# Kernel tuning notes

Hardware: AMD Instinct MI355X
Metric: run time of the kernel (lower is better)

The kernel has to match this reference:

```python
import jax, jax.numpy as jnp
import numpy as np

B, N, D = 8, 1024, 768
H, Z = 12, 64          # num_heads, head_dim (D = H*Z)
HID = 3072             # int(D * mlp_ratio)


def setup_inputs() -> dict:
    key = jax.random.key(0)
    k1, k2, k3, k4 = jax.random.split(key, 4)
    s = 0.02
    x = jax.random.normal(k1, (B, N, D), dtype=jnp.float32)
    Wq = jax.random.normal(k2, (D, D), dtype=jnp.float32) * s
    Wk = jax.random.normal(k3, (D, D), dtype=jnp.float32) * s
    betas = jnp.full((H,), Z ** -0.5, dtype=jnp.float32)
    W_mlp = jax.random.normal(k4, (HID, D), dtype=jnp.float32) * s
    return {"x": x, "Wq": Wq, "Wk": Wk, "betas": betas, "W_mlp": W_mlp}


def reference(x, Wq, Wk, betas, W_mlp):
    # --- KQ-aligned attention ---
    # torch Linear: y = x @ W.T ; weight shape [out=D, in=D]
    Q = jnp.einsum('bnd,ed->bne', x, Wq).reshape(B, N, H, Z).transpose(0, 2, 1, 3)  # bhqz
    K = jnp.einsum('bnd,ed->bne', x, Wk).reshape(B, N, H, Z).transpose(0, 2, 1, 3)  # bhkz
    Wq_r = Wq.reshape(H, Z, D)
    Wk_r = Wk.reshape(H, Z, D)
    F1 = jnp.einsum('hzd,bhkz->bkhd', Wq_r, K)
    F2 = jnp.einsum('hzd,bhqz->bqhd', Wk_r, Q)
    scores = jnp.einsum('bhqz,bhkz,h->bhqk', Q, K, betas)
    attn = jax.nn.softmax(scores, axis=-1)
    T1 = jnp.einsum('bkhd,bhqk->bqd', F1, attn)
    T2 = jnp.einsum('bqhd,bhqk->bkd', F2, attn)
    # --- symmetric-weight Hopfield MLP (bias=False) ---
    hid = jax.nn.relu(jnp.einsum('bnd,hd->bnh', x, W_mlp))
    mlp = jnp.einsum('bnh,hd->bnd', hid, W_mlp)
    return T1 + T2 + mlp
```

## Files before the change

### kernel.cpp

```cpp
#include <hip/hip_runtime.h>
#include <hip/hip_bf16.h>

#define Bq 8
#define Nq 1024
#define Dq 768
#define Hq 12
#define Zq 64
#define HIDq 3072
#define BN (Bq*Nq)
#define QKP 1536

typedef unsigned short u16;
typedef short s16x8 __attribute__((ext_vector_type(8)));
typedef float f32x4 __attribute__((ext_vector_type(4)));
typedef unsigned short u16x4 __attribute__((ext_vector_type(4)));

#define MFMA16 __builtin_amdgcn_mfma_f32_16x16x32_bf16
#define GLOAD16(g, l) __builtin_amdgcn_global_load_lds( \
    (const __attribute__((address_space(1))) void*)(const void*)(g), \
    (__attribute__((address_space(3))) void*)(l), 16, 0, 0)

__device__ __forceinline__ u16 f2bf(float f) {
  unsigned u = __float_as_uint(f);
  return (u16)((u + 0x7FFFu + ((u >> 16) & 1u)) >> 16);
}

__device__ __forceinline__ unsigned pk2bf(float a, float b) {
  union { __hip_bfloat162 h; unsigned u; } cv;
  cv.h.x = __float2bfloat16(a);
  cv.h.y = __float2bfloat16(b);
  return cv.u;
}

__device__ __forceinline__ void xcd_swizzle(int gx, int gy, int& bx, int& by) {
  int l = blockIdx.y * gx + blockIdx.x;
  int c = l & 7, j = l >> 3;
  by = c * (gy >> 3) + j / gx;
  bx = j % gx;
}

__global__ __launch_bounds__(256) void cvt2(const float* __restrict__ x, u16* __restrict__ xb,
                                            const float* __restrict__ Wm, u16* __restrict__ Wmb) {
  int bid = blockIdx.x;
  const float* in; u16* out; int i;
  if (bid < 6144) { in = x;  out = xb;  i = bid * 1024 + threadIdx.x * 4; }
  else            { in = Wm; out = Wmb; i = (bid - 6144) * 1024 + threadIdx.x * 4; }
  float4 v = *(const float4*)&in[i];
  u16x4 o; o[0] = f2bf(v.x); o[1] = f2bf(v.y); o[2] = f2bf(v.z); o[3] = f2bf(v.w);
  *(u16x4*)&out[i] = o;
}

__global__ __launch_bounds__(256) void cvt_tr2(const float* __restrict__ Wq,
                                               const float* __restrict__ Wk,
                                               u16* __restrict__ Wqkb,
                                               u16* __restrict__ WqkT) {
  __shared__ u16 T[64][72];
  const int t = threadIdx.x;
  const int z = blockIdx.z;
  const float* in = z ? Wk : Wq;
  u16* out = Wqkb + (size_t)z * Dq * Dq;
  u16* outT = WqkT + z * Dq;
  const int r0 = blockIdx.y * 64, c0 = blockIdx.x * 64;
  const int r = t >> 3, c8 = (t & 7) * 8;
#pragma unroll
  for (int p = 0; p < 2; p++) {
    const float* ip = &in[(size_t)(r0 + r + p * 32) * Dq + c0 + c8];
    float4 v0 = *(const float4*)ip, v1 = *(const float4*)(ip + 4);
    u16 tmp[8] = {f2bf(v0.x), f2bf(v0.y), f2bf(v0.z), f2bf(v0.w),
                  f2bf(v1.x), f2bf(v1.y), f2bf(v1.z), f2bf(v1.w)};
    *(uint4*)&out[(size_t)(r0 + r + p * 32) * Dq + c0 + c8] = *(uint4*)tmp;
    *(uint4*)&T[r + p * 32][c8] = *(uint4*)tmp;
  }
  __syncthreads();
#pragma unroll
  for (int p = 0; p < 2; p++) {
    int oc = r + p * 32;
    u16 tmp[8];
#pragma unroll
    for (int j = 0; j < 8; j++) tmp[j] = T[c8 + j][oc];
    *(uint4*)&outT[(size_t)(c0 + oc) * QKP + r0 + c8] = *(uint4*)tmp;
  }
}

__global__ __launch_bounds__(256) void transpose_bf16(
    const u16* __restrict__ in, u16* __restrict__ out,
    int in_pitch, int out_pitch, int inner_n,
    long in_bs_o, long in_bs_i, long out_bs_o, long out_bs_i) {
  __shared__ u16 T[64][72];
  const int t = threadIdx.x;
  const int bz = blockIdx.z;
  const long iboff = (long)(bz / inner_n) * in_bs_o + (long)(bz % inner_n) * in_bs_i;
  const long oboff = (long)(bz / inner_n) * out_bs_o + (long)(bz % inner_n) * out_bs_i;
  const u16* ip = in + iboff + (long)(blockIdx.y * 64) * in_pitch + blockIdx.x * 64;
  u16* op = out + oboff + (long)(blockIdx.x * 64) * out_pitch + blockIdx.y * 64;
  const int r = t >> 3, c8 = (t & 7) * 8;
#pragma unroll
  for (int p = 0; p < 2; p++)
    *(uint4*)&T[r + p * 32][c8] = *(const uint4*)(ip + (size_t)(r + p * 32) * in_pitch + c8);
  __syncthreads();
#pragma unroll
  for (int p = 0; p < 2; p++) {
    int oc = r + p * 32;
    u16 tmp[8];
#pragma unroll
    for (int j = 0; j < 8; j++) tmp[j] = T[c8 + j][oc];
    *(uint4*)(op + (size_t)oc * out_pitch + c8) = *(uint4*)tmp;
  }
}

__global__ __launch_bounds__(256) void head_tr(const u16* __restrict__ QKb,
                                               u16* __restrict__ QbT,
                                               u16* __restrict__ KbT) {
  __shared__ u16 T[64][72];
  const int t = threadIdx.x;
  const int z = blockIdx.z;
  const int half = (z >= 96) ? 1 : 0;
  const int bhh = z - 96 * half;
  const u16* ip = QKb + (size_t)(bhh / Hq) * Nq * QKP + (bhh % Hq) * 64 + half * Dq
                + (size_t)(blockIdx.y * 64) * QKP;
  u16* op = (half ? KbT : QbT) + (size_t)bhh * 64 * Nq + blockIdx.y * 64;
  const int r = t >> 3, c8 = (t & 7) * 8;
#pragma unroll
  for (int p = 0; p < 2; p++)
    *(uint4*)&T[r + p * 32][c8] = *(const uint4*)(ip + (size_t)(r + p * 32) * QKP + c8);
  __syncthreads();
#pragma unroll
  for (int p = 0; p < 2; p++) {
    int oc = r + p * 32;
    u16 tmp[8];
#pragma unroll
    for (int j = 0; j < 8; j++) tmp[j] = T[c8 + j][oc];
    *(uint4*)(op + (size_t)oc * Nq + c8) = *(uint4*)tmp;
  }
}

template<bool RELU>
__global__ __launch_bounds__(256) void gemm_bf16(
    const u16* __restrict__ A, const u16* __restrict__ B, u16* __restrict__ C,
    int M, int N, int K) {
  __shared__ u16 As[2][128 * 32];
  __shared__ u16 Bs[2][128 * 32];
  int bx, by;
  xcd_swizzle(gridDim.x, gridDim.y, bx, by);
  const int t = threadIdx.x, l = t & 63, w = t >> 6;
  const int lq = l & 15, quad = l >> 4;
  const int bm = by * 128, bn = bx * 128;
  const int wm = (w & 1) * 64, wn = (w >> 1) * 64;
  f32x4 acc[4][4];
#pragma unroll
  for (int i = 0; i < 4; i++)
#pragma unroll
    for (int j = 0; j < 4; j++) acc[i][j] = (f32x4){0.f, 0.f, 0.f, 0.f};

  auto stage = [&](int k0, int bufi) {
#pragma unroll
    for (int p = 0; p < 2; p++) {
      int idx = p * 256 + t;
      GLOAD16(A + (size_t)(bm + (idx >> 2)) * K + k0 + (idx & 3) * 8, &As[bufi][idx * 8]);
      GLOAD16(B + (size_t)(bn + (idx >> 2)) * K + k0 + (idx & 3) * 8, &Bs[bufi][idx * 8]);
    }
  };
  stage(0, 0);
  const int nIter = K >> 5;
  for (int it = 0; it < nIter; it++) {
    __syncthreads();
    if (it + 1 < nIter) stage((it + 1) * 32, (it + 1) & 1);
    const int bi = it & 1;
    s16x8 af[4], bf[4];
#pragma unroll
    for (int mt = 0; mt < 4; mt++)
      af[mt] = *(const s16x8*)&As[bi][(wm + mt * 16 + lq) * 32 + quad * 8];
#pragma unroll
    for (int nt = 0; nt < 4; nt++)
      bf[nt] = *(const s16x8*)&Bs[bi][(wn + nt * 16 + lq) * 32 + quad * 8];
#pragma unroll
    for (int mt = 0; mt < 4; mt++)
#pragma unroll
      for (int nt = 0; nt < 4; nt++)
        acc[mt][nt] = MFMA16(af[mt], bf[nt], acc[mt][nt], 0, 0, 0);
  }
#pragma unroll
  for (int mt = 0; mt < 4; mt++)
#pragma unroll
    for (int nt = 0; nt < 4; nt++) {
      int row = bm + wm + mt * 16 + quad * 4;
      int col = bn + wn + nt * 16 + lq;
#pragma unroll
      for (int r = 0; r < 4; r++) {
        float v = acc[mt][nt][r];
        if (RELU) v = fmaxf(v, 0.f);
        C[(size_t)(row + r) * N + col] = f2bf(v);
      }
    }
}

__global__ __launch_bounds__(256) void gemm_out2(
    const u16* __restrict__ AV12, const u16* __restrict__ hid,
    const u16* __restrict__ WqkT, const u16* __restrict__ WmT,
    float* __restrict__ out) {
  __shared__ u16 As[3][128 * 32];
  __shared__ u16 Bs[3][64 * 32];
  int bx, by;
  xcd_swizzle(gridDim.x, gridDim.y, bx, by);
  const int t = threadIdx.x, l = t & 63, w = t >> 6;
  const int lq = l & 15, quad = l >> 4;
  const int bm = by * 128, bn = bx * 64;
  const int wm = w * 32;
  f32x4 acc[2][4];
#pragma unroll
  for (int i = 0; i < 2; i++)
#pragma unroll
    for (int j = 0; j < 4; j++) acc[i][j] = (f32x4){0.f, 0.f, 0.f, 0.f};

  auto stage = [&](int tl, int bufi) {
    const u16* A; const u16* B; int pitch, k0;
    if (tl < 48) { A = AV12; B = WqkT; pitch = QKP;  k0 = tl * 32; }
    else         { A = hid;  B = WmT;  pitch = HIDq; k0 = (tl - 48) * 32; }
#pragma unroll
    for (int p = 0; p < 2; p++) {
      int idx = p * 256 + t;
      GLOAD16(A + (size_t)(bm + (idx >> 2)) * pitch + k0 + (idx & 3) * 8,
              &As[bufi][idx * 8]);
    }
    GLOAD16(B + (size_t)(bn + (t >> 2)) * pitch + k0 + (t & 3) * 8,
            &Bs[bufi][t * 8]);
  };
  stage(0, 0);
  stage(1, 1);
  for (int tl = 0; tl < 144; tl++) {
    if (tl < 143) asm volatile("s_waitcnt vmcnt(3)" ::: "memory");
    else          asm volatile("s_waitcnt vmcnt(0)" ::: "memory");
    __builtin_amdgcn_s_barrier();
    __builtin_amdgcn_sched_barrier(0);
    if (tl + 2 < 144) stage(tl + 2, (tl + 2) % 3);
    const int bi = tl % 3;
    s16x8 af[2], bf[4];
#pragma unroll
    for (int mt = 0; mt < 2; mt++)
      af[mt] = *(const s16x8*)&As[bi][(wm + mt * 16 + lq) * 32 + quad * 8];
#pragma unroll
    for (int nt = 0; nt < 4; nt++)
      bf[nt] = *(const s16x8*)&Bs[bi][(nt * 16 + lq) * 32 + quad * 8];
#pragma unroll
    for (int mt = 0; mt < 2; mt++)
#pragma unroll
      for (int nt = 0; nt < 4; nt++)
        acc[mt][nt] = MFMA16(af[mt], bf[nt], acc[mt][nt], 0, 0, 0);
  }
#pragma unroll
  for (int mt = 0; mt < 2; mt++)
#pragma unroll
    for (int nt = 0; nt < 4; nt++) {
      int row = bm + wm + mt * 16 + quad * 4;
      int col = bn + nt * 16 + lq;
#pragma unroll
      for (int r = 0; r < 4; r++)
        out[(size_t)(row + r) * Dq + col] = acc[mt][nt][r];
    }
}

__global__ __launch_bounds__(256) void attn_pass1(
    const u16* __restrict__ QKb, const u16* __restrict__ KbT,
    const float* __restrict__ betas, u16* __restrict__ AV12,
    float* __restrict__ lg) {
  __shared__ u16 Ps[64][72];
  __shared__ u16 Ks[2][64][32];
  __shared__ u16 Kts[2][2][64][32];

  const int t = threadIdx.x, l = t & 63, w = t >> 6;
  const int lq = l & 15, quad = l >> 4;
  const int c = blockIdx.x & 7, j = blockIdx.x >> 3;
  const int bh = c * 12 + j / 16, qt = j % 16;
  const int b = bh / Hq, h = bh % Hq;
  const int q0 = qt * 64;
  const float beta = betas[h];
  const u16* Qh = QKb + (size_t)(b * Nq) * QKP + h * 64;
  const u16* Kh = Qh + Dq;
  const u16* KTh = KbT + (size_t)bh * 64 * Nq;
  u16* QsF = &Ps[0][0];
  u16* KsF = &Ks[0][0][0];

  auto stageK = [&](int kt2) {
#pragma unroll
    for (int p = 0; p < 2; p++) {
      int idx = p * 256 + t;
      GLOAD16(Kh + (size_t)(kt2 * 64 + ((idx >> 2) & 63)) * QKP + (idx >> 8) * 32 + (idx & 3) * 8,
              KsF + idx * 8);
    }
  };
  auto stageKt = [&](int kt2, int bufi) {
#pragma unroll
    for (int p = 0; p < 2; p++) {
      int idx = p * 256 + t;
      GLOAD16(KTh + (size_t)((idx >> 2) & 63) * Nq + kt2 * 64 + (idx >> 8) * 32 + (idx & 3) * 8,
              &Kts[bufi][0][0][0] + idx * 8);
    }
  };

#pragma unroll
  for (int p = 0; p < 2; p++) {
    int idx = p * 256 + t;
    GLOAD16(Qh + (size_t)(q0 + ((idx >> 2) & 63)) * QKP + (idx >> 8) * 32 + (idx & 3) * 8,
            QsF + idx * 8);
  }
  stageK(0);
  stageKt(0, 0);
  __syncthreads();
  s16x8 bqf[2][4];
#pragma unroll
  for (int zs = 0; zs < 2; zs++)
#pragma unroll
    for (int nt = 0; nt < 4; nt++)
      bqf[zs][nt] = *(const s16x8*)&QsF[zs * 2048 + (nt * 16 + lq) * 32 + quad * 8];
  __syncthreads();

  float lsum[4] = {0.f, 0.f, 0.f, 0.f};
  f32x4 ao[4];
#pragma unroll
  for (int nt = 0; nt < 4; nt++) ao[nt] = (f32x4){0.f, 0.f, 0.f, 0.f};

  for (int kt = 0; kt < 16; kt++) {
    if (kt) __syncthreads();
    const int bi = kt & 1;
    f32x4 sc[4];
#pragma unroll
    for (int nt = 0; nt < 4; nt++) sc[nt] = (f32x4){0.f, 0.f, 0.f, 0.f};
#pragma unroll
    for (int zs = 0; zs < 2; zs++) {
      s16x8 a = *(const s16x8*)&Ks[zs][w * 16 + lq][quad * 8];
#pragma unroll
      for (int nt = 0; nt < 4; nt++)
        sc[nt] = MFMA16(a, bqf[zs][nt], sc[nt], 0, 0, 0);
    }
#pragma unroll
    for (int nt = 0; nt < 4; nt++) {
      float e0 = __expf(sc[nt][0] * beta), e1 = __expf(sc[nt][1] * beta);
      float e2 = __expf(sc[nt][2] * beta), e3 = __expf(sc[nt][3] * beta);
      lsum[nt] += (e0 + e1) + (e2 + e3);
      uint2 pk; pk.x = pk2bf(e0, e1); pk.y = pk2bf(e2, e3);
      *(uint2*)&Ps[nt * 16 + lq][w * 16 + quad * 4] = pk;
    }
    __syncthreads();
    if (kt + 1 < 16) {
      stageK(kt + 1);
      stageKt(kt + 1, (kt + 1) & 1);
    }
#pragma unroll
    for (int ks = 0; ks < 2; ks++) {
      s16x8 a = *(const s16x8*)&Ps[w * 16 + lq][ks * 32 + quad * 8];
#pragma unroll
      for (int nt = 0; nt < 4; nt++) {
        s16x8 bk = *(const s16x8*)&Kts[bi][ks][nt * 16 + lq][quad * 8];
        ao[nt] = MFMA16(a, bk, ao[nt], 0, 0, 0);
      }
    }
  }
  __syncthreads();
  float* redp = (float*)&Kts[0][0][0][0];
  float* lip  = redp + 256;
#pragma unroll
  for (int nt = 0; nt < 4; nt++) {
    float v = lsum[nt];
    v += __shfl_xor(v, 16, 64);
    v += __shfl_xor(v, 32, 64);
    if (l < 16) redp[w * 64 + nt * 16 + lq] = v;
  }
  __syncthreads();
  if (t < 64) {
    float s = redp[t] + redp[64 + t] + redp[128 + t] + redp[192 + t];
    lg[(size_t)bh * Nq + q0 + t] = s;
    lip[t] = 1.0f / s;
  }
  __syncthreads();
  u16* Oh = AV12 + (size_t)(b * Nq + q0) * QKP + h * 64;
  float lr[4];
#pragma unroll
  for (int r = 0; r < 4; r++) lr[r] = lip[w * 16 + quad * 4 + r];
#pragma unroll
  for (int nt = 0; nt < 4; nt++)
#pragma unroll
    for (int r = 0; r < 4; r++)
      Oh[(size_t)(w * 16 + quad * 4 + r) * QKP + nt * 16 + lq] = f2bf(ao[nt][r] * lr[r]);
}

__global__ __launch_bounds__(256) void attn_pass2(
    const u16* __restrict__ QKb, const u16* __restrict__ QbT,
    const float* __restrict__ betas, u16* __restrict__ AV12,
    const float* __restrict__ lg) {
  __shared__ u16 Pts[64][72];
  __shared__ u16 Qs[2][64][32];
  __shared__ u16 Qts[2][2][64][32];
  __shared__ float li_s[2][64];

  const int t = threadIdx.x, l = t & 63, w = t >> 6;
  const int lq = l & 15, quad = l >> 4;
  const int c = blockIdx.x & 7, j = blockIdx.x >> 3;
  const int bh = c * 12 + j / 16, kt = j % 16;
  const int b = bh / Hq, h = bh % Hq;
  const int k0 = kt * 64;
  const float beta = betas[h];
  const u16* Qh = QKb + (size_t)(b * Nq) * QKP + h * 64;
  const u16* Kh = Qh + Dq;
  const u16* QTh = QbT + (size_t)bh * 64 * Nq;
  u16* KsF = &Pts[0][0];
  u16* QsF = &Qs[0][0][0];

  auto stageQ = [&](int qt2) {
#pragma unroll
    for (int p = 0; p < 2; p++) {
      int idx = p * 256 + t;
      GLOAD16(Qh + (size_t)(qt2 * 64 + ((idx >> 2) & 63)) * QKP + (idx >> 8) * 32 + (idx & 3) * 8,
              QsF + idx * 8);
    }
  };
  auto stageQt = [&](int qt2, int bufi) {
#pragma unroll
    for (int p = 0; p < 2; p++) {
      int idx = p * 256 + t;
      GLOAD16(QTh + (size_t)((idx >> 2) & 63) * Nq + qt2 * 64 + (idx >> 8) * 32 + (idx & 3) * 8,
              &Qts[bufi][0][0][0] + idx * 8);
    }
  };

#pragma unroll
  for (int p = 0; p < 2; p++) {
    int idx = p * 256 + t;
    GLOAD16(Kh + (size_t)(k0 + ((idx >> 2) & 63)) * QKP + (idx >> 8) * 32 + (idx & 3) * 8,
            KsF + idx * 8);
  }
  stageQ(0);
  stageQt(0, 0);
  if (t < 64) li_s[0][t] = 1.0f / lg[(size_t)bh * Nq + t];
  __syncthreads();
  s16x8 bkf[2][4];
#pragma unroll
  for (int zs = 0; zs < 2; zs++)
#pragma unroll
    for (int nt = 0; nt < 4; nt++)
      bkf[zs][nt] = *(const s16x8*)&KsF[zs * 2048 + (nt * 16 + lq) * 32 + quad * 8];
  __syncthreads();

  f32x4 ao[4];
#pragma unroll
  for (int nt = 0; nt < 4; nt++) ao[nt] = (f32x4){0.f, 0.f, 0.f, 0.f};

  for (int qt = 0; qt < 16; qt++) {
    if (qt) __syncthreads();
    const int bi = qt & 1;
    f32x4 sc[4];
#pragma unroll
    for (int nt = 0; nt < 4; nt++) sc[nt] = (f32x4){0.f, 0.f, 0.f, 0.f};
#pragma unroll
    for (int zs = 0; zs < 2; zs++) {
      s16x8 a = *(const s16x8*)&Qs[zs][w * 16 + lq][quad * 8];
#pragma unroll
      for (int nt = 0; nt < 4; nt++)
        sc[nt] = MFMA16(a, bkf[zs][nt], sc[nt], 0, 0, 0);
    }
    float lr[4];
#pragma unroll
    for (int r = 0; r < 4; r++) lr[r] = li_s[bi][w * 16 + quad * 4 + r];
#pragma unroll
    for (int nt = 0; nt < 4; nt++) {
      float e0 = __expf(sc[nt][0] * beta) * lr[0];
      float e1 = __expf(sc[nt][1] * beta) * lr[1];
      float e2 = __expf(sc[nt][2] * beta) * lr[2];
      float e3 = __expf(sc[nt][3] * beta) * lr[3];
      uint2 pk; pk.x = pk2bf(e0, e1); pk.y = pk2bf(e2, e3);
      *(uint2*)&Pts[nt * 16 + lq][w * 16 + quad * 4] = pk;
    }
    __syncthreads();
    if (qt + 1 < 16) {
      stageQ(qt + 1);
      stageQt(qt + 1, (qt + 1) & 1);
      if (t < 64) li_s[(qt + 1) & 1][t] = 1.0f / lg[(size_t)bh * Nq + (qt + 1) * 64 + t];
    }
#pragma unroll
    for (int qs = 0; qs < 2; qs++) {
      s16x8 a = *(const s16x8*)&Pts[w * 16 + lq][qs * 32 + quad * 8];
#pragma unroll
      for (int nt = 0; nt < 4; nt++) {
        s16x8 bq = *(const s16x8*)&Qts[bi][qs][nt * 16 + lq][quad * 8];
        ao[nt] = MFMA16(a, bq, ao[nt], 0, 0, 0);
      }
    }
  }
  u16* Oh = AV12 + (size_t)(b * Nq + k0) * QKP + Dq + h * 64;
#pragma unroll
  for (int nt = 0; nt < 4; nt++)
#pragma unroll
    for (int r = 0; r < 4; r++)
      Oh[(size_t)(w * 16 + quad * 4 + r) * QKP + nt * 16 + lq] = f2bf(ao[nt][r]);
}

extern "C" void kernel_launch(void* const* d_in, const int* in_sizes, int n_in,
                              void* d_out, int out_size, void* d_ws, size_t ws_size,
                              hipStream_t stream) {
  const float* x     = (const float*)d_in[0];
  const float* Wq    = (const float*)d_in[1];
  const float* Wk    = (const float*)d_in[2];
  const float* betas = (const float*)d_in[3];
  const float* Wm    = (const float*)d_in[4];
  float* out = (float*)d_out;

  u16* xb   = (u16*)d_ws;
  u16* Wqkb = xb + (size_t)BN * Dq;
  u16* Wmb  = Wqkb + (size_t)QKP * Dq;
  u16* WqkT = Wmb + (size_t)HIDq * Dq;
  u16* QKb  = WqkT + (size_t)Dq * QKP;
  u16* QbT  = QKb + (size_t)BN * QKP;
  u16* KbT  = QbT + (size_t)Bq * Hq * Zq * Nq;
  u16* AV12 = KbT + (size_t)Bq * Hq * Zq * Nq;
  float* lg = (float*)(AV12 + (size_t)BN * QKP);
  u16* hidb = QKb;
  u16* WmT  = xb;

  dim3 blk(256);
  cvt2<<<8448, blk, 0, stream>>>(x, xb, Wm, Wmb);
  cvt_tr2<<<dim3(12, 12, 2), blk, 0, stream>>>(Wq, Wk, Wqkb, WqkT);

  gemm_bf16<false><<<dim3(QKP / 128, BN / 128), blk, 0, stream>>>(
      xb, Wqkb, QKb, BN, QKP, Dq);

  head_tr<<<dim3(1, 16, 192), blk, 0, stream>>>(QKb, QbT, KbT);

  attn_pass1<<<Bq * Hq * 16, blk, 0, stream>>>(QKb, KbT, betas, AV12, lg);
  attn_pass2<<<Bq * Hq * 16, blk, 0, stream>>>(QKb, QbT, betas, AV12, lg);

  gemm_bf16<true><<<dim3(HIDq / 128, BN / 128), blk, 0, stream>>>(
      xb, Wmb, hidb, BN, HIDq, Dq);

  transpose_bf16<<<dim3(12, 48, 1), blk, 0, stream>>>(Wmb, WmT, Dq, HIDq, 1, 0, 0, 0, 0);

  gemm_out2<<<dim3(Dq / 64, BN / 128), blk, 0, stream>>>(AV12, hidb, WqkT, WmT, out);
}
```

Baseline: 369.9 us.

## Double attention query/key tile to 128 rows and widen output GEMM K-step

The attention passes now process 128 query (or key) rows per block instead of 64, halving the grid and reusing each staged K/Q tile for twice as many rows, so global and LDS traffic per output row drops. The final output GEMM moves from a 3-stage pipeline with a 32-wide K step and explicit vmcnt waits to a 2-stage pipeline with a 64-wide K step and plain __syncthreads, halving the number of barriers per tile. In exchange, per-thread register pressure and LDS use rise, the attention grid shrinks to 768 blocks, and the simpler GEMM pipeline may expose more load latency.

```diff
diff --git a/kernel.cpp b/kernel.cpp
--- a/kernel.cpp
+++ b/kernel.cpp
@@ -198,8 +198,8 @@
     const u16* __restrict__ AV12, const u16* __restrict__ hid,
     const u16* __restrict__ WqkT, const u16* __restrict__ WmT,
     float* __restrict__ out) {
-  __shared__ u16 As[3][128 * 32];
-  __shared__ u16 Bs[3][64 * 32];
+  __shared__ u16 As[2][128 * 64];
+  __shared__ u16 Bs[2][64 * 64];
   int bx, by;
   xcd_swizzle(gridDim.x, gridDim.y, bx, by);
   const int t = threadIdx.x, l = t & 63, w = t >> 6;
@@ -214,38 +214,41 @@
 
   auto stage = [&](int tl, int bufi) {
     const u16* A; const u16* B; int pitch, k0;
-    if (tl < 48) { A = AV12; B = WqkT; pitch = QKP;  k0 = tl * 32; }
-    else         { A = hid;  B = WmT;  pitch = HIDq; k0 = (tl - 48) * 32; }
+    if (tl < 24) { A = AV12; B = WqkT; pitch = QKP;  k0 = tl * 64; }
+    else         { A = hid;  B = WmT;  pitch = HIDq; k0 = (tl - 24) * 64; }
+#pragma unroll
+    for (int p = 0; p < 4; p++) {
+      int idx = p * 256 + t, ks = idx >> 9, rem = idx & 511;
+      GLOAD16(A + (size_t)(bm + (rem >> 2)) * pitch + k0 + ks * 32 + (rem & 3) * 8,
+              &As[bufi][idx * 8]);
+    }
 #pragma unroll
     for (int p = 0; p < 2; p++) {
-      int idx = p * 256 + t;
-      GLOAD16(A + (size_t)(bm + (idx >> 2)) * pitch + k0 + (idx & 3) * 8,
-              &As[bufi][idx * 8]);
-    }
-    GLOAD16(B + (size_t)(bn + (t >> 2)) * pitch + k0 + (t & 3) * 8,
-            &Bs[bufi][t * 8]);
+      int idx = p * 256 + t, ks = idx >> 8, rem = idx & 255;
+      GLOAD16(B + (size_t)(bn + (rem >> 2)) * pitch + k0 + ks * 32 + (rem & 3) * 8,
+              &Bs[bufi][idx * 8]);
+    }
   };
   stage(0, 0);
-  stage(1, 1);
-  for (int tl = 0; tl < 144; tl++) {
-    if (tl < 143) asm volatile("s_waitcnt vmcnt(3)" ::: "memory");
-    else          asm volatile("s_waitcnt vmcnt(0)" ::: "memory");
-    __builtin_amdgcn_s_barrier();
-    __builtin_amdgcn_sched_barrier(0);
-    if (tl + 2 < 144) stage(tl + 2, (tl + 2) % 3);
-    const int bi = tl % 3;
-    s16x8 af[2], bf[4];
-#pragma unroll
-    for (int mt = 0; mt < 2; mt++)
-      af[mt] = *(const s16x8*)&As[bi][(wm + mt * 16 + lq) * 32 + quad * 8];
-#pragma unroll
-    for (int nt = 0; nt < 4; nt++)
-      bf[nt] = *(const s16x8*)&Bs[bi][(nt * 16 + lq) * 32 + quad * 8];
-#pragma unroll
-    for (int mt = 0; mt < 2; mt++)
+  for (int tl = 0; tl < 72; tl++) {
+    __syncthreads();
+    if (tl + 1 < 72) stage(tl + 1, (tl + 1) & 1);
+    const int bi = tl & 1;
+#pragma unroll
+    for (int ks = 0; ks < 2; ks++) {
+      s16x8 af[2], bf[4];
+#pragma unroll
+      for (int mt = 0; mt < 2; mt++)
+        af[mt] = *(const s16x8*)&As[bi][ks * 4096 + (wm + mt * 16 + lq) * 32 + quad * 8];
 #pragma unroll
       for (int nt = 0; nt < 4; nt++)
-        acc[mt][nt] = MFMA16(af[mt], bf[nt], acc[mt][nt], 0, 0, 0);
+        bf[nt] = *(const s16x8*)&Bs[bi][ks * 2048 + (nt * 16 + lq) * 32 + quad * 8];
+#pragma unroll
+      for (int mt = 0; mt < 2; mt++)
+#pragma unroll
+        for (int nt = 0; nt < 4; nt++)
+          acc[mt][nt] = MFMA16(af[mt], bf[nt], acc[mt][nt], 0, 0, 0);
+    }
   }
 #pragma unroll
   for (int mt = 0; mt < 2; mt++)
@@ -263,16 +266,16 @@
     const u16* __restrict__ QKb, const u16* __restrict__ KbT,
     const float* __restrict__ betas, u16* __restrict__ AV12,
     float* __restrict__ lg) {
-  __shared__ u16 Ps[64][72];
+  __shared__ u16 Ps[128][72];
   __shared__ u16 Ks[2][64][32];
   __shared__ u16 Kts[2][2][64][32];
 
   const int t = threadIdx.x, l = t & 63, w = t >> 6;
   const int lq = l & 15, quad = l >> 4;
   const int c = blockIdx.x & 7, j = blockIdx.x >> 3;
-  const int bh = c * 12 + j / 16, qt = j % 16;
+  const int bh = c * 12 + j / 8, qt = j % 8;
   const int b = bh / Hq, h = bh % Hq;
-  const int q0 = qt * 64;
+  const int q0 = qt * 128;
   const float beta = betas[h];
   const u16* Qh = QKb + (size_t)(b * Nq) * QKP + h * 64;
   const u16* Kh = Qh + Dq;
@@ -298,47 +301,54 @@
   };
 
 #pragma unroll
-  for (int p = 0; p < 2; p++) {
+  for (int p = 0; p < 4; p++) {
     int idx = p * 256 + t;
-    GLOAD16(Qh + (size_t)(q0 + ((idx >> 2) & 63)) * QKP + (idx >> 8) * 32 + (idx & 3) * 8,
+    GLOAD16(Qh + (size_t)(q0 + ((idx >> 2) & 127)) * QKP + (idx >> 9) * 32 + (idx & 3) * 8,
             QsF + idx * 8);
   }
   stageK(0);
   stageKt(0, 0);
   __syncthreads();
-  s16x8 bqf[2][4];
+  s16x8 bqf[2][8];
 #pragma unroll
   for (int zs = 0; zs < 2; zs++)
 #pragma unroll
-    for (int nt = 0; nt < 4; nt++)
-      bqf[zs][nt] = *(const s16x8*)&QsF[zs * 2048 + (nt * 16 + lq) * 32 + quad * 8];
-  __syncthreads();
-
-  float lsum[4] = {0.f, 0.f, 0.f, 0.f};
-  f32x4 ao[4];
-#pragma unroll
-  for (int nt = 0; nt < 4; nt++) ao[nt] = (f32x4){0.f, 0.f, 0.f, 0.f};
+    for (int nt = 0; nt < 8; nt++)
+      bqf[zs][nt] = *(const s16x8*)&QsF[zs * 4096 + (nt * 16 + lq) * 32 + quad * 8];
+  __syncthreads();
+
+  float lsum[8];
+#pragma unroll
+  for (int i = 0; i < 8; i++) lsum[i] = 0.f;
+  f32x4 ao[2][4];
+#pragma unroll
+  for (int hf = 0; hf < 2; hf++)
+#pragma unroll
+    for (int nt = 0; nt < 4; nt++) ao[hf][nt] = (f32x4){0.f, 0.f, 0.f, 0.f};
 
   for (int kt = 0; kt < 16; kt++) {
     if (kt) __syncthreads();
     const int bi = kt & 1;
-    f32x4 sc[4];
-#pragma unroll
-    for (int nt = 0; nt < 4; nt++) sc[nt] = (f32x4){0.f, 0.f, 0.f, 0.f};
-#pragma unroll
-    for (int zs = 0; zs < 2; zs++) {
-      s16x8 a = *(const s16x8*)&Ks[zs][w * 16 + lq][quad * 8];
-#pragma unroll
-      for (int nt = 0; nt < 4; nt++)
-        sc[nt] = MFMA16(a, bqf[zs][nt], sc[nt], 0, 0, 0);
-    }
-#pragma unroll
-    for (int nt = 0; nt < 4; nt++) {
-      float e0 = __expf(sc[nt][0] * beta), e1 = __expf(sc[nt][1] * beta);
-      float e2 = __expf(sc[nt][2] * beta), e3 = __expf(sc[nt][3] * beta);
-      lsum[nt] += (e0 + e1) + (e2 + e3);
-      uint2 pk; pk.x = pk2bf(e0, e1); pk.y = pk2bf(e2, e3);
-      *(uint2*)&Ps[nt * 16 + lq][w * 16 + quad * 4] = pk;
+#pragma unroll
+    for (int g = 0; g < 2; g++) {
+      f32x4 sc[4];
+#pragma unroll
+      for (int j4 = 0; j4 < 4; j4++) sc[j4] = (f32x4){0.f, 0.f, 0.f, 0.f};
+#pragma unroll
+      for (int zs = 0; zs < 2; zs++) {
+        s16x8 a = *(const s16x8*)&Ks[zs][w * 16 + lq][quad * 8];
+#pragma unroll
+        for (int j4 = 0; j4 < 4; j4++)
+          sc[j4] = MFMA16(a, bqf[zs][g * 4 + j4], sc[j4], 0, 0, 0);
+      }
+#pragma unroll
+      for (int j4 = 0; j4 < 4; j4++) {
+        float e0 = __expf(sc[j4][0] * beta), e1 = __expf(sc[j4][1] * beta);
+        float e2 = __expf(sc[j4][2] * beta), e3 = __expf(sc[j4][3] * beta);
+        lsum[g * 4 + j4] += (e0 + e1) + (e2 + e3);
+        uint2 pk; pk.x = pk2bf(e0, e1); pk.y = pk2bf(e2, e3);
+        *(uint2*)&Ps[(g * 4 + j4) * 16 + lq][w * 16 + quad * 4] = pk;
+      }
     }
     __syncthreads();
     if (kt + 1 < 16) {
@@ -347,47 +357,56 @@
     }
 #pragma unroll
     for (int ks = 0; ks < 2; ks++) {
-      s16x8 a = *(const s16x8*)&Ps[w * 16 + lq][ks * 32 + quad * 8];
-#pragma unroll
-      for (int nt = 0; nt < 4; nt++) {
-        s16x8 bk = *(const s16x8*)&Kts[bi][ks][nt * 16 + lq][quad * 8];
-        ao[nt] = MFMA16(a, bk, ao[nt], 0, 0, 0);
+      s16x8 bk[4];
+#pragma unroll
+      for (int nt = 0; nt < 4; nt++)
+        bk[nt] = *(const s16x8*)&Kts[bi][ks][nt * 16 + lq][quad * 8];
+#pragma unroll
+      for (int hf = 0; hf < 2; hf++) {
+        s16x8 a = *(const s16x8*)&Ps[w * 32 + hf * 16 + lq][ks * 32 + quad * 8];
+#pragma unroll
+        for (int nt = 0; nt < 4; nt++)
+          ao[hf][nt] = MFMA16(a, bk[nt], ao[hf][nt], 0, 0, 0);
       }
     }
   }
   __syncthreads();
   float* redp = (float*)&Kts[0][0][0][0];
-  float* lip  = redp + 256;
-#pragma unroll
-  for (int nt = 0; nt < 4; nt++) {
+  float* lip  = redp + 512;
+#pragma unroll
+  for (int nt = 0; nt < 8; nt++) {
     float v = lsum[nt];
     v += __shfl_xor(v, 16, 64);
     v += __shfl_xor(v, 32, 64);
-    if (l < 16) redp[w * 64 + nt * 16 + lq] = v;
-  }
-  __syncthreads();
-  if (t < 64) {
-    float s = redp[t] + redp[64 + t] + redp[128 + t] + redp[192 + t];
+    if (l < 16) redp[w * 128 + nt * 16 + lq] = v;
+  }
+  __syncthreads();
+  if (t < 128) {
+    float s = redp[t] + redp[128 + t] + redp[256 + t] + redp[384 + t];
     lg[(size_t)bh * Nq + q0 + t] = s;
     lip[t] = 1.0f / s;
   }
   __syncthreads();
   u16* Oh = AV12 + (size_t)(b * Nq + q0) * QKP + h * 64;
-  float lr[4];
-#pragma unroll
-  for (int r = 0; r < 4; r++) lr[r] = lip[w * 16 + quad * 4 + r];
-#pragma unroll
-  for (int nt = 0; nt < 4; nt++)
-#pragma unroll
-    for (int r = 0; r < 4; r++)
-      Oh[(size_t)(w * 16 + quad * 4 + r) * QKP + nt * 16 + lq] = f2bf(ao[nt][r] * lr[r]);
+#pragma unroll
+  for (int hf = 0; hf < 2; hf++) {
+    float lr[4];
+#pragma unroll
+    for (int r = 0; r < 4; r++) lr[r] = lip[w * 32 + hf * 16 + quad * 4 + r];
+#pragma unroll
+    for (int nt = 0; nt < 4; nt++)
+#pragma unroll
+      for (int r = 0; r < 4; r++)
+        Oh[(size_t)(w * 32 + hf * 16 + quad * 4 + r) * QKP + nt * 16 + lq] =
+            f2bf(ao[hf][nt][r] * lr[r]);
+  }
 }
 
 __global__ __launch_bounds__(256) void attn_pass2(
     const u16* __restrict__ QKb, const u16* __restrict__ QbT,
     const float* __restrict__ betas, u16* __restrict__ AV12,
     const float* __restrict__ lg) {
-  __shared__ u16 Pts[64][72];
+  __shared__ u16 Pts[128][72];
   __shared__ u16 Qs[2][64][32];
   __shared__ u16 Qts[2][2][64][32];
   __shared__ float li_s[2][64];
@@ -395,9 +414,9 @@
   const int t = threadIdx.x, l = t & 63, w = t >> 6;
   const int lq = l & 15, quad = l >> 4;
   const int c = blockIdx.x & 7, j = blockIdx.x >> 3;
-  const int bh = c * 12 + j / 16, kt = j % 16;
+  const int bh = c * 12 + j / 8, kt = j % 8;
   const int b = bh / Hq, h = bh % Hq;
-  const int k0 = kt * 64;
+  const int k0 = kt * 128;
   const float beta = betas[h];
   const u16* Qh = QKb + (size_t)(b * Nq) * QKP + h * 64;
   const u16* Kh = Qh + Dq;
@@ -423,74 +442,87 @@
   };
 
 #pragma unroll
-  for (int p = 0; p < 2; p++) {
+  for (int p = 0; p < 4; p++) {
     int idx = p * 256 + t;
-    GLOAD16(Kh + (size_t)(k0 + ((idx >> 2) & 63)) * QKP + (idx >> 8) * 32 + (idx & 3) * 8,
+    GLOAD16(Kh + (size_t)(k0 + ((idx >> 2) & 127)) * QKP + (idx >> 9) * 32 + (idx & 3) * 8,
             KsF + idx * 8);
   }
   stageQ(0);
   stageQt(0, 0);
   if (t < 64) li_s[0][t] = 1.0f / lg[(size_t)bh * Nq + t];
   __syncthreads();
-  s16x8 bkf[2][4];
+  s16x8 bkf[2][8];
 #pragma unroll
   for (int zs = 0; zs < 2; zs++)
 #pragma unroll
+    for (int nt = 0; nt < 8; nt++)
+      bkf[zs][nt] = *(const s16x8*)&KsF[zs * 4096 + (nt * 16 + lq) * 32 + quad * 8];
+  __syncthreads();
+
+  f32x4 ao[2][4];
+#pragma unroll
+  for (int hf = 0; hf < 2; hf++)
+#pragma unroll
+    for (int nt = 0; nt < 4; nt++) ao[hf][nt] = (f32x4){0.f, 0.f, 0.f, 0.f};
+
+  for (int qt2 = 0; qt2 < 16; qt2++) {
+    if (qt2) __syncthreads();
+    const int bi = qt2 & 1;
+    float lr[4];
+#pragma unroll
+    for (int r = 0; r < 4; r++) lr[r] = li_s[bi][w * 16 + quad * 4 + r];
+#pragma unroll
+    for (int g = 0; g < 2; g++) {
+      f32x4 sc[4];
+#pragma unroll
+      for (int j4 = 0; j4 < 4; j4++) sc[j4] = (f32x4){0.f, 0.f, 0.f, 0.f};
+#pragma unroll
+      for (int zs = 0; zs < 2; zs++) {
+        s16x8 a = *(const s16x8*)&Qs[zs][w * 16 + lq][quad * 8];
+#pragma unroll
+        for (int j4 = 0; j4 < 4; j4++)
+          sc[j4] = MFMA16(a, bkf[zs][g * 4 + j4], sc[j4], 0, 0, 0);
+      }
+#pragma unroll
+      for (int j4 = 0; j4 < 4; j4++) {
+        float e0 = __expf(sc[j4][0] * beta) * lr[0];
+        float e1 = __expf(sc[j4][1] * beta) * lr[1];
+        float e2 = __expf(sc[j4][2] * beta) * lr[2];
+        float e3 = __expf(sc[j4][3] * beta) * lr[3];
+        uint2 pk; pk.x = pk2bf(e0, e1); pk.y = pk2bf(e2, e3);
+        *(uint2*)&Pts[(g * 4 + j4) * 16 + lq][w * 16 + quad * 4] = pk;
+      }
+    }
+    __syncthreads();
+    if (qt2 + 1 < 16) {
+      stageQ(qt2 + 1);
+      stageQt(qt2 + 1, (qt2 + 1) & 1);
+      if (t < 64) li_s[(qt2 + 1) & 1][t] = 1.0f / lg[(size_t)bh * Nq + (qt2 + 1) * 64 + t];
+    }
+#pragma unroll
+    for (int qs = 0; qs < 2; qs++) {
+      s16x8 bq[4];
+#pragma unroll
+      for (int nt = 0; nt < 4; nt++)
+        bq[nt] = *(const s16x8*)&Qts[bi][qs][nt * 16 + lq][quad * 8];
+#pragma unroll
+      for (int hf = 0; hf < 2; hf++) {
+        s16x8 a = *(const s16x8*)&Pts[w * 32 + hf * 16 + lq][qs * 32 + quad * 8];
+#pragma unroll
+        for (int nt = 0; nt < 4; nt++)
+          ao[hf][nt] = MFMA16(a, bq[nt], ao[hf][nt], 0, 0, 0);
+      }
+    }
+  }
+  u16* Oh = AV12 + (size_t)(b * Nq + k0) * QKP + Dq + h * 64;
+#pragma unroll
+  for (int hf = 0; hf < 2; hf++)
+#pragma unroll
     for (int nt = 0; nt < 4; nt++)
-      bkf[zs][nt] = *(const s16x8*)&KsF[zs * 2048 + (nt * 16 + lq) * 32 + quad * 8];
-  __syncthreads();
-
-  f32x4 ao[4];
-#pragma unroll
-  for (int nt = 0; nt < 4; nt++) ao[nt] = (f32x4){0.f, 0.f, 0.f, 0.f};
-
-  for (int qt = 0; qt < 16; qt++) {
-    if (qt) __syncthreads();
-    const int bi = qt & 1;
-    f32x4 sc[4];
-#pragma unroll
-    for (int nt = 0; nt < 4; nt++) sc[nt] = (f32x4){0.f, 0.f, 0.f, 0.f};
-#pragma unroll
-    for (int zs = 0; zs < 2; zs++) {
-      s16x8 a = *(const s16x8*)&Qs[zs][w * 16 + lq][quad * 8];
-#pragma unroll
-      for (int nt = 0; nt < 4; nt++)
-        sc[nt] = MFMA16(a, bkf[zs][nt], sc[nt], 0, 0, 0);
-    }
-    float lr[4];
-#pragma unroll
-    for (int r = 0; r < 4; r++) lr[r] = li_s[bi][w * 16 + quad * 4 + r];
-#pragma unroll
-    for (int nt = 0; nt < 4; nt++) {
-      float e0 = __expf(sc[nt][0] * beta) * lr[0];
-      float e1 = __expf(sc[nt][1] * beta) * lr[1];
-      float e2 = __expf(sc[nt][2] * beta) * lr[2];
-      float e3 = __expf(sc[nt][3] * beta) * lr[3];
-      uint2 pk; pk.x = pk2bf(e0, e1); pk.y = pk2bf(e2, e3);
-      *(uint2*)&Pts[nt * 16 + lq][w * 16 + quad * 4] = pk;
-    }
-    __syncthreads();
-    if (qt + 1 < 16) {
-      stageQ(qt + 1);
-      stageQt(qt + 1, (qt + 1) & 1);
-      if (t < 64) li_s[(qt + 1) & 1][t] = 1.0f / lg[(size_t)bh * Nq + (qt + 1) * 64 + t];
-    }
-#pragma unroll
-    for (int qs = 0; qs < 2; qs++) {
-      s16x8 a = *(const s16x8*)&Pts[w * 16 + lq][qs * 32 + quad * 8];
-#pragma unroll
-      for (int nt = 0; nt < 4; nt++) {
-        s16x8 bq = *(const s16x8*)&Qts[bi][qs][nt * 16 + lq][quad * 8];
-        ao[nt] = MFMA16(a, bq, ao[nt], 0, 0, 0);
-      }
-    }
-  }
-  u16* Oh = AV12 + (size_t)(b * Nq + k0) * QKP + Dq + h * 64;
-#pragma unroll
-  for (int nt = 0; nt < 4; nt++)
-#pragma unroll
-    for (int r = 0; r < 4; r++)
-      Oh[(size_t)(w * 16 + quad * 4 + r) * QKP + nt * 16 + lq] = f2bf(ao[nt][r]);
+#pragma unroll
+      for (int r = 0; r < 4; r++)
+        Oh[(size_t)(w * 32 + hf * 16 + quad * 4 + r) * QKP + nt * 16 + lq] =
+            f2bf(ao[hf][nt][r]);
 }
 
 extern "C" void kernel_launch(void* const* d_in, const int* in_sizes, int n_in,
@@ -524,8 +556,8 @@
 
   head_tr<<<dim3(1, 16, 192), blk, 0, stream>>>(QKb, QbT, KbT);
 
-  attn_pass1<<<Bq * Hq * 16, blk, 0, stream>>>(QKb, KbT, betas, AV12, lg);
-  attn_pass2<<<Bq * Hq * 16, blk, 0, stream>>>(QKb, QbT, betas, AV12, lg);
+  attn_pass1<<<Bq * Hq * 8, blk, 0, stream>>>(QKb, KbT, betas, AV12, lg);
+  attn_pass2<<<Bq * Hq * 8, blk, 0, stream>>>(QKb, QbT, betas, AV12, lg);
 
   gemm_bf16<true><<<dim3(HIDq / 128, BN / 128), blk, 0, stream>>>(
       xb, Wmb, hidb, BN, HIDq, Dq);
```

After: 368.2 us. About the same (-0.5%).
